# Kernel optimization log

Measured on AMD Instinct MI355X. Metric: run time of the kernel, lower is better.

The kernel has to match this reference:

```python
import jax, jax.numpy as jnp
import numpy as np

COMMITMENT_COST = 0.25


def setup_inputs() -> dict:
    key = jax.random.key(0)
    k1, k2 = jax.random.split(key)
    B, S, D, K = 64, 2048, 256, 1024
    inputs = jax.random.normal(k1, (B, S, D), dtype=jnp.float32)
    codebook = jax.random.normal(k2, (K, D), dtype=jnp.float32)
    return {"inputs": inputs, "codebook": codebook}


def reference(inputs, codebook):
    # inputs: [B, S, D], codebook: [K, D]
    D = inputs.shape[-1]
    K = codebook.shape[0]
    flat = inputs.reshape(-1, D)                                  # [N, D]
    distances = (jnp.sum(flat * flat, axis=1, keepdims=True)
                 + jnp.sum(codebook * codebook, axis=1)
                 - 2.0 * jnp.matmul(flat, codebook.T))
    encoding_indices = jnp.argmin(distances, axis=1)               # [N]
    # one-hot @ codebook  ==  gather rows
    quantized = codebook[encoding_indices].reshape(inputs.shape)   # [B, S, D]

    q_sg = jax.lax.stop_gradient(quantized)
    x_sg = jax.lax.stop_gradient(inputs)
    e_latent_loss = jnp.mean((q_sg - inputs) ** 2)
    q_latent_loss = jnp.mean((quantized - x_sg) ** 2)
    loss = q_latent_loss + COMMITMENT_COST * e_latent_loss

    # straight-through estimator
    quantized_st = inputs + jax.lax.stop_gradient(quantized - inputs)

    # perplexity from code usage histogram
    N = flat.shape[0]
    counts = jnp.zeros((K,), dtype=jnp.float32).at[encoding_indices].add(1.0)
    avg_probs = counts / N
    perplexity = jnp.exp(-jnp.sum(avg_probs * jnp.log(avg_probs + 1e-10)))

    return (quantized_st,
            encoding_indices.reshape(inputs.shape[:-1]),
            loss,
            perplexity)
```

## Files before the change

kernel.cpp:

```cpp
#include <hip/hip_runtime.h>
#include <cfloat>

#define DD 256
#define KK 1024
#define NROWS 131072
#define QELEMS 33554432
#define ROWS_PB 64
#define THETA 12.0f
#define CAND_MAX 16

typedef __attribute__((ext_vector_type(8))) short bf16x8;
typedef __attribute__((ext_vector_type(16))) float f32x16;

__device__ inline unsigned short rne_bf16(float f) {
    unsigned u = __float_as_uint(f);
    unsigned r = (u + 0x7fffu + ((u >> 16) & 1u)) >> 16;
    return (unsigned short)r;
}
__device__ inline unsigned fenc(float f) {
    unsigned u = __float_as_uint(f);
    return (u & 0x80000000u) ? ~u : (u | 0x80000000u);
}
__device__ inline float fdec(unsigned e) {
    return (e & 0x80000000u) ? __uint_as_float(e & 0x7fffffffu)
                             : __uint_as_float(~e);
}

__global__ void k_rowsq(const float* __restrict__ src, float* __restrict__ dst,
                        int nrows) {
#pragma clang fp contract(off)
    const int lane = threadIdx.x & 63;
    const int wid = (blockIdx.x * blockDim.x + threadIdx.x) >> 6;
    if (wid >= nrows) return;
    float r = 0.0f;
    if (lane < 16) {
        const int half = lane >> 3, j = lane & 7;
        const float* a = src + (size_t)wid * DD + half * 128 + j;
        float v = a[0];
        r = v * v;
        for (int t = 1; t < 16; ++t) {
            float u = a[8 * t];
            float p = u * u;
            r = r + p;
        }
    }
    float o1 = __shfl_xor(r, 1); r = r + o1;
    float o2 = __shfl_xor(r, 2); r = r + o2;
    float o4 = __shfl_xor(r, 4); r = r + o4;
    float o8 = __shfl_xor(r, 8); r = r + o8;
    if (lane == 0) dst[wid] = r;
}

__global__ void k_prep(const float* __restrict__ cb,
                       unsigned short* __restrict__ cbh,
                       int* __restrict__ hist, float* __restrict__ lossAcc) {
    const int code = blockIdx.x, k = threadIdx.x;
    cbh[(size_t)(k >> 3) * 8192 + code * 8 + (k & 7)] = rne_bf16(cb[code * DD + k]);
    if (code == 0) {
        for (int i = k; i < KK; i += 256) hist[i] = 0;
        if (k == 0) *lossAcc = 0.0f;
    }
}

__global__ __launch_bounds__(512, 2) void k2_gemm(
    const float* __restrict__ x, const unsigned short* __restrict__ cbh,
    const float* __restrict__ c2, int* __restrict__ candBuf) {
    __shared__ unsigned short aL[16384];
    __shared__ unsigned short bL[16384];
    __shared__ unsigned wmin[64];
    __shared__ int ccnt[64];
    __shared__ unsigned short clist[64][CAND_MAX];

    const int tid = threadIdx.x;
    const int lane = tid & 63;
    const int w = tid >> 6;
    const int row0 = blockIdx.x * 64;
    const int h = lane >> 5;
    const int l31 = lane & 31;

    if (tid < 64) { wmin[tid] = 0xFFFFFFFFu; ccnt[tid] = 0; }

    {
        const float4* xg = (const float4*)(x + (size_t)row0 * DD);
#pragma unroll
        for (int i = 0; i < 8; ++i) {
            int lin = tid + i * 512;
            int r = lin >> 6, c4 = lin & 63;
            float4 v = xg[lin];
            unsigned p0 = (unsigned)rne_bf16(v.x) | ((unsigned)rne_bf16(v.y) << 16);
            unsigned p1 = (unsigned)rne_bf16(v.z) | ((unsigned)rne_bf16(v.w) << 16);
            unsigned short* p = &aL[(c4 >> 1) * 512 + r * 8 + (c4 & 1) * 4];
            *(uint2*)p = make_uint2(p0, p1);
        }
    }

    const bf16x8* cb8 = (const bf16x8*)cbh;
    bf16x8 st0 = cb8[tid], st1 = cb8[tid + 512],
           st2 = cb8[tid + 1024], st3 = cb8[tid + 1536];
    __syncthreads();
    {
        bf16x8* bw = (bf16x8*)bL;
        bw[tid] = st0; bw[tid + 512] = st1;
        bw[tid + 1024] = st2; bw[tid + 1536] = st3;
    }
    __syncthreads();

    f32x16 acc[2][4];
#pragma unroll
    for (int rf = 0; rf < 2; ++rf)
#pragma unroll
        for (int cf = 0; cf < 4; ++cf)
#pragma unroll
            for (int e = 0; e < 16; ++e) acc[rf][cf][e] = 0.0f;

    const int aoff0 = l31 * 8;
    const int aoff1 = (32 + l31) * 8;
    const int boff = h * 8192 + (w * 128 + l31) * 8;

    for (int ks = 0; ks < 16; ++ks) {
        if (ks < 15) {
            int base = (ks + 1) * 2048 + tid;
            st0 = cb8[base]; st1 = cb8[base + 512];
            st2 = cb8[base + 1024]; st3 = cb8[base + 1536];
        }
        const int ab = (2 * ks + h) * 512;
        bf16x8 av0 = *(const bf16x8*)(&aL[ab + aoff0]);
        bf16x8 av1 = *(const bf16x8*)(&aL[ab + aoff1]);
#pragma unroll
        for (int cf = 0; cf < 4; ++cf) {
            bf16x8 bv = *(const bf16x8*)(&bL[boff + cf * 256]);
            acc[0][cf] = __builtin_amdgcn_mfma_f32_32x32x16_bf16(av0, bv, acc[0][cf], 0, 0, 0);
            acc[1][cf] = __builtin_amdgcn_mfma_f32_32x32x16_bf16(av1, bv, acc[1][cf], 0, 0, 0);
        }
        __syncthreads();
        if (ks < 15) {
            bf16x8* bw = (bf16x8*)bL;
            bw[tid] = st0; bw[tid + 512] = st1;
            bw[tid + 1024] = st2; bw[tid + 1536] = st3;
            __syncthreads();
        }
    }

    float c2v[4];
#pragma unroll
    for (int cf = 0; cf < 4; ++cf) c2v[cf] = c2[w * 128 + cf * 32 + l31];
#pragma unroll
    for (int rf = 0; rf < 2; ++rf)
#pragma unroll
        for (int cf = 0; cf < 4; ++cf)
#pragma unroll
            for (int e = 0; e < 16; ++e)
                acc[rf][cf][e] = fmaf(-2.0f, acc[rf][cf][e], c2v[cf]);

#pragma unroll
    for (int rf = 0; rf < 2; ++rf)
#pragma unroll
        for (int r = 0; r < 16; ++r) {
            float v = fminf(fminf(acc[rf][0][r], acc[rf][1][r]),
                            fminf(acc[rf][2][r], acc[rf][3][r]));
            v = fminf(v, __shfl_xor(v, 1));
            v = fminf(v, __shfl_xor(v, 2));
            v = fminf(v, __shfl_xor(v, 4));
            v = fminf(v, __shfl_xor(v, 8));
            v = fminf(v, __shfl_xor(v, 16));
            if (l31 == 0)
                atomicMin(&wmin[rf * 32 + (r & 3) + 8 * (r >> 2) + 4 * h], fenc(v));
        }
    __syncthreads();

#pragma unroll
    for (int rf = 0; rf < 2; ++rf)
#pragma unroll
        for (int r = 0; r < 16; ++r) {
            int rr = rf * 32 + (r & 3) + 8 * (r >> 2) + 4 * h;
            float gm = fdec(wmin[rr]) + THETA;
#pragma unroll
            for (int cf = 0; cf < 4; ++cf) {
                if (acc[rf][cf][r] <= gm) {
                    int pos = atomicAdd(&ccnt[rr], 1);
                    if (pos < CAND_MAX)
                        clist[rr][pos] = (unsigned short)(w * 128 + cf * 32 + l31);
                }
            }
        }
    __syncthreads();

    if (tid < 64) {
        int* o = candBuf + (size_t)(row0 + tid) * (CAND_MAX + 1);
        o[0] = ccnt[tid];
#pragma unroll
        for (int i = 0; i < CAND_MAX; ++i) o[1 + i] = clist[tid][i];
    }
}

__global__ __launch_bounds__(256) void k_recheck(
    const float* __restrict__ x, const float* __restrict__ cb,
    const float* __restrict__ c2, const int* __restrict__ candBuf,
    float* __restrict__ outIdx, int* __restrict__ hist,
    float* __restrict__ lossAcc) {
#pragma clang fp contract(off)
    __shared__ float xsT[DD * 65];
    __shared__ float x2s[64];
    __shared__ unsigned bestS[64];
    __shared__ int bestK[64];
    __shared__ int wl[64 * CAND_MAX];
    __shared__ float wls[64 * CAND_MAX];
    __shared__ int ovf[64];
    __shared__ int wln, ovfn;

    const int tid = threadIdx.x;
    const int row0 = blockIdx.x * 64;

    if (tid < 64) { bestS[tid] = 0xFFFFFFFFu; bestK[tid] = 0x7fffffff; }
    if (tid == 0) { wln = 0; ovfn = 0; }

    {
        const float4* xg = (const float4*)(x + (size_t)row0 * DD);
#pragma unroll
        for (int i = 0; i < 16; ++i) {
            int lin = tid + i * 256;
            int r = lin >> 6, c4 = lin & 63;
            float4 v = xg[lin];
            xsT[(c4 * 4 + 0) * 65 + r] = v.x;
            xsT[(c4 * 4 + 1) * 65 + r] = v.y;
            xsT[(c4 * 4 + 2) * 65 + r] = v.z;
            xsT[(c4 * 4 + 3) * 65 + r] = v.w;
        }
    }
    __syncthreads();

    if (tid < 64) {
        const int row = tid;
        float hsum[2];
#pragma unroll
        for (int hh = 0; hh < 2; ++hh) {
            float a[8];
#pragma unroll
            for (int j = 0; j < 8; ++j) {
                float v = xsT[(hh * 128 + j) * 65 + row];
                a[j] = v * v;
            }
            for (int t = 1; t < 16; ++t) {
#pragma unroll
                for (int j = 0; j < 8; ++j) {
                    float u = xsT[(hh * 128 + j + 8 * t) * 65 + row];
                    float p = u * u;
                    a[j] = a[j] + p;
                }
            }
            float s01 = a[0] + a[1], s23 = a[2] + a[3];
            float s45 = a[4] + a[5], s67 = a[6] + a[7];
            hsum[hh] = (s01 + s23) + (s45 + s67);
        }
        x2s[row] = hsum[0] + hsum[1];

        const int* cd = candBuf + (size_t)(row0 + row) * (CAND_MAX + 1);
        int n = cd[0];
        if (n <= CAND_MAX) {
            int base = atomicAdd(&wln, n);
            for (int i = 0; i < n; ++i) wl[base + i] = (row << 16) | cd[1 + i];
        } else {
            ovf[atomicAdd(&ovfn, 1)] = row;
        }
    }
    __syncthreads();

    const int NW = wln;
    const int NO = ovfn;

    for (int it = tid; it < NW; it += 256) {
        const int row = wl[it] >> 16, k = wl[it] & 0xFFFF;
        const float* cr = cb + (size_t)k * DD;
        float dot = 0.0f;
#pragma unroll 8
        for (int d = 0; d < DD; ++d)
            dot = fmaf(xsT[d * 65 + row], cr[d], dot);
        float T1 = x2s[row] + c2[k];
        float s = fmaf(-2.0f, dot, T1);
        wls[it] = s;
        atomicMin(&bestS[row], fenc(s));
    }
    __syncthreads();

    for (int it = tid; it < NW; it += 256) {
        const int row = wl[it] >> 16, k = wl[it] & 0xFFFF;
        if (fenc(wls[it]) == bestS[row]) atomicMin(&bestK[row], k);
    }

    for (int o = 0; o < NO; ++o) {
        __syncthreads();
        const int row = ovf[o];
        float myS[4];
#pragma unroll
        for (int q = 0; q < 4; ++q) {
            const int k = tid + q * 256;
            const float* cr = cb + (size_t)k * DD;
            float dot = 0.0f;
#pragma unroll 8
            for (int d = 0; d < DD; ++d)
                dot = fmaf(xsT[d * 65 + row], cr[d], dot);
            float T1 = x2s[row] + c2[k];
            myS[q] = fmaf(-2.0f, dot, T1);
            atomicMin(&bestS[row], fenc(myS[q]));
        }
        __syncthreads();
#pragma unroll
        for (int q = 0; q < 4; ++q)
            if (fenc(myS[q]) == bestS[row]) atomicMin(&bestK[row], tid + q * 256);
    }
    __syncthreads();

    if (tid < 64) {
        const float bs = fdec(bestS[tid]);
        const int bk = bestK[tid];
        outIdx[row0 + tid] = (float)bk;
        atomicAdd(hist + bk, 1);
        float ls = bs;
#pragma unroll
        for (int off = 32; off > 0; off >>= 1) ls += __shfl_down(ls, off);
        if (tid == 0) atomicAdd(lossAcc, ls);
    }
}

__global__ __launch_bounds__(256) void k3_gather(
    const float* __restrict__ cb, const float* __restrict__ outIdx,
    float* __restrict__ outQ) {
    __shared__ int sidx[ROWS_PB];
    const int t = threadIdx.x;
    const int row0 = blockIdx.x * ROWS_PB;
    if (t < ROWS_PB) sidx[t] = (int)outIdx[row0 + t];
    __syncthreads();

    float4* q4 = (float4*)(outQ + (size_t)row0 * DD);
    const float4* c4 = (const float4*)cb;
#pragma unroll
    for (int i = 0; i < 16; ++i) {
        int lin = t + i * 256;
        int r = lin >> 6;
        int c = lin & 63;
        q4[lin] = c4[(size_t)sidx[r] * 64 + c];
    }
}

__global__ void k4_final(const int* __restrict__ hist,
                         const float* __restrict__ lossAcc,
                         float* __restrict__ outLoss,
                         float* __restrict__ outPerp) {
    __shared__ float red[256];
    const int t = threadIdx.x;
    float e = 0.0f;
    for (int i = t; i < KK; i += 256) {
        float p = (float)hist[i] * (1.0f / (float)NROWS);
        e -= p * logf(p + 1e-10f);
    }
    red[t] = e;
    __syncthreads();
    for (int s = 128; s > 0; s >>= 1) {
        if (t < s) red[t] += red[t + s];
        __syncthreads();
    }
    if (t == 0) {
        *outPerp = expf(red[0]);
        *outLoss = 1.25f * (*lossAcc) / (float)QELEMS;
    }
}

extern "C" void kernel_launch(void* const* d_in, const int* in_sizes, int n_in,
                              void* d_out, int out_size, void* d_ws, size_t ws_size,
                              hipStream_t stream) {
    const float* x = (const float*)d_in[0];
    const float* cb = (const float*)d_in[1];

    float* outQ = (float*)d_out;
    float* outIdx = outQ + QELEMS;
    float* outLoss = outIdx + NROWS;
    float* outPerp = outLoss + 1;

    unsigned short* cbh = (unsigned short*)d_ws;
    float* c2 = (float*)((char*)d_ws + 524288);
    int* hist = (int*)(c2 + KK);
    float* lossAcc = (float*)(hist + KK);
    int* candBuf = (int*)outQ;

    k_rowsq<<<dim3(KK / 4), dim3(256), 0, stream>>>(cb, c2, KK);
    k_prep<<<dim3(KK), dim3(256), 0, stream>>>(cb, cbh, hist, lossAcc);
    k2_gemm<<<dim3(NROWS / 64), dim3(512), 0, stream>>>(x, cbh, c2, candBuf);
    k_recheck<<<dim3(NROWS / 64), dim3(256), 0, stream>>>(x, cb, c2, candBuf,
                                                          outIdx, hist, lossAcc);
    k3_gather<<<dim3(NROWS / ROWS_PB), dim3(256), 0, stream>>>(cb, outIdx, outQ);
    k4_final<<<dim3(1), dim3(256), 0, stream>>>(hist, lossAcc, outLoss, outPerp);
}
```

Baseline: 553.7 us.

## Load codebook fragments directly from global into registers, drop LDS staging

Removes the shared-memory B tile and its per-step barriers. Each wave now loads its bf16 codebook fragments straight from global (L2-resident) memory into registers, double-buffered two k-steps ahead, with the loop fully unrolled. This removes the LDS writes, LDS reads and __syncthreads from the inner loop and frees 32KB of LDS, which may allow more blocks per CU. In exchange every wave issues more global loads, since B is no longer shared across the block, and the code relies on the cache and register prefetch to hide latency.

```diff
diff --git a/kernel.cpp b/kernel.cpp
--- a/kernel.cpp
+++ b/kernel.cpp
@@ -66,7 +66,6 @@
     const float* __restrict__ x, const unsigned short* __restrict__ cbh,
     const float* __restrict__ c2, int* __restrict__ candBuf) {
     __shared__ unsigned short aL[16384];
-    __shared__ unsigned short bL[16384];
     __shared__ unsigned wmin[64];
     __shared__ int ccnt[64];
     __shared__ unsigned short clist[64][CAND_MAX];
@@ -93,16 +92,6 @@
             *(uint2*)p = make_uint2(p0, p1);
         }
     }
-
-    const bf16x8* cb8 = (const bf16x8*)cbh;
-    bf16x8 st0 = cb8[tid], st1 = cb8[tid + 512],
-           st2 = cb8[tid + 1024], st3 = cb8[tid + 1536];
-    __syncthreads();
-    {
-        bf16x8* bw = (bf16x8*)bL;
-        bw[tid] = st0; bw[tid + 512] = st1;
-        bw[tid + 1024] = st2; bw[tid + 1536] = st3;
-    }
     __syncthreads();
 
     f32x16 acc[2][4];
@@ -113,33 +102,40 @@
 #pragma unroll
             for (int e = 0; e < 16; ++e) acc[rf][cf][e] = 0.0f;
 
-    const int aoff0 = l31 * 8;
-    const int aoff1 = (32 + l31) * 8;
-    const int boff = h * 8192 + (w * 128 + l31) * 8;
-
-    for (int ks = 0; ks < 16; ++ks) {
-        if (ks < 15) {
-            int base = (ks + 1) * 2048 + tid;
-            st0 = cb8[base]; st1 = cb8[base + 512];
-            st2 = cb8[base + 1024]; st3 = cb8[base + 1536];
-        }
-        const int ab = (2 * ks + h) * 512;
-        bf16x8 av0 = *(const bf16x8*)(&aL[ab + aoff0]);
-        bf16x8 av1 = *(const bf16x8*)(&aL[ab + aoff1]);
+    const bf16x8* aptr = (const bf16x8*)aL + h * 64 + l31;
+    const bf16x8* bptr = (const bf16x8*)cbh + (size_t)h * 1024 + w * 128 + l31;
+
+    bf16x8 b0[4], b1[4];
+#define LDB(KS, B)                                                            \
+    do {                                                                      \
+        B[0] = bptr[(KS) * 2048];                                             \
+        B[1] = bptr[(KS) * 2048 + 32];                                        \
+        B[2] = bptr[(KS) * 2048 + 64];                                        \
+        B[3] = bptr[(KS) * 2048 + 96];                                        \
+    } while (0)
+
+    LDB(0, b0);
+    LDB(1, b1);
+#pragma unroll
+    for (int ks = 0; ks < 16; ks += 2) {
+        bf16x8 av0 = aptr[ks * 128];
+        bf16x8 av1 = aptr[ks * 128 + 32];
 #pragma unroll
         for (int cf = 0; cf < 4; ++cf) {
-            bf16x8 bv = *(const bf16x8*)(&bL[boff + cf * 256]);
-            acc[0][cf] = __builtin_amdgcn_mfma_f32_32x32x16_bf16(av0, bv, acc[0][cf], 0, 0, 0);
-            acc[1][cf] = __builtin_amdgcn_mfma_f32_32x32x16_bf16(av1, bv, acc[1][cf], 0, 0, 0);
-        }
-        __syncthreads();
-        if (ks < 15) {
-            bf16x8* bw = (bf16x8*)bL;
-            bw[tid] = st0; bw[tid + 512] = st1;
-            bw[tid + 1024] = st2; bw[tid + 1536] = st3;
-            __syncthreads();
-        }
-    }
+            acc[0][cf] = __builtin_amdgcn_mfma_f32_32x32x16_bf16(av0, b0[cf], acc[0][cf], 0, 0, 0);
+            acc[1][cf] = __builtin_amdgcn_mfma_f32_32x32x16_bf16(av1, b0[cf], acc[1][cf], 0, 0, 0);
+        }
+        if (ks + 2 < 16) LDB(ks + 2, b0);
+        bf16x8 aw0 = aptr[(ks + 1) * 128];
+        bf16x8 aw1 = aptr[(ks + 1) * 128 + 32];
+#pragma unroll
+        for (int cf = 0; cf < 4; ++cf) {
+            acc[0][cf] = __builtin_amdgcn_mfma_f32_32x32x16_bf16(aw0, b1[cf], acc[0][cf], 0, 0, 0);
+            acc[1][cf] = __builtin_amdgcn_mfma_f32_32x32x16_bf16(aw1, b1[cf], acc[1][cf], 0, 0, 0);
+        }
+        if (ks + 3 < 16) LDB(ks + 3, b1);
+    }
+#undef LDB
 
     float c2v[4];
 #pragma unroll
```

After: 536.6 us. -3.1%, faster.
